# Optimization experiments

Measured on AMD Instinct MI355X. Metric: run time of the kernel, lower is better.

## Reference

```python
import jax, jax.numpy as jnp
import numpy as np

N = 100000
IN_DIM = 512
HID = (256, 256, 128)
NNZ = 3200000
SLOPE = 0.25  # leaky_relu negative slope


def _spmm(rows, cols, vals, X):
    # out[i] = sum_{e: rows[e]==i} vals[e] * X[cols[e]]  -> sparse [N,N] @ X
    return jax.ops.segment_sum(vals[:, None] * X[cols], rows, num_segments=N)


def setup_inputs() -> dict:
    key = jax.random.key(0)
    ks = jax.random.split(key, 10)
    x = jax.random.normal(ks[0], (N, IN_DIM), dtype=jnp.float32)
    adj_rows = jax.random.randint(ks[1], (NNZ,), 0, N, dtype=jnp.int32)
    adj_cols = jax.random.randint(ks[2], (NNZ,), 0, N, dtype=jnp.int32)
    adj_vals = jax.random.uniform(ks[3], (NNZ,), dtype=jnp.float32)
    # xavier_normal-ish init for weights, zeros for biases
    def xav(k, fan_in, fan_out):
        std = (2.0 / (fan_in + fan_out)) ** 0.5
        return std * jax.random.normal(k, (fan_in, fan_out), dtype=jnp.float32)
    W1 = xav(ks[4], IN_DIM, HID[0]); b1 = jnp.zeros((HID[0],), jnp.float32)
    W2 = xav(ks[5], HID[0], HID[1]); b2 = jnp.zeros((HID[1],), jnp.float32)
    W3 = xav(ks[6], HID[1], HID[2]); b3 = jnp.zeros((HID[2],), jnp.float32)
    return {"x": x, "adj_rows": adj_rows, "adj_cols": adj_cols, "adj_vals": adj_vals,
            "W1": W1, "b1": b1, "W2": W2, "b2": b2, "W3": W3, "b3": b3}


def reference(x, adj_rows, adj_cols, adj_vals, W1, b1, W2, b2, W3, b3):
    # Inference mode: F.dropout with training=False is identity.
    def layer(h, W, b):
        support = h @ W                       # dense GEMM [N, d_out]
        out = _spmm(adj_rows, adj_cols, adj_vals, support) + b
        return jax.nn.leaky_relu(out, SLOPE)
    h = layer(x, W1, b1)
    h = layer(h, W2, b2)
    h = layer(h, W3, b3)
    return h
```

## Files before the change

kernel.cpp:

```cpp
#include <hip/hip_runtime.h>

#define N_NODES 100000
#define NNZ_E   3200000
#define SLOPE   0.25f

#define NBUCK 782
#define PBLK  512
#define PCH   6250
#define CAP   6144

typedef __attribute__((ext_vector_type(8))) short bf16x8;
typedef __attribute__((ext_vector_type(4))) float f32x4;

__device__ __forceinline__ unsigned short f2b(float f) {
    union { float f; unsigned int u; } c; c.f = f;
    unsigned int u = c.u + 0x7fffu + ((c.u >> 16) & 1u);
    return (unsigned short)(u >> 16);
}
__device__ __forceinline__ float b2f_lo(unsigned int u) {
    union { unsigned int u; float f; } c; c.u = u << 16; return c.f;
}
__device__ __forceinline__ float b2f_hi(unsigned int u) {
    union { unsigned int u; float f; } c; c.u = u & 0xffff0000u; return c.f;
}

__device__ __forceinline__ void load_lds16(const unsigned short* gp, unsigned short* lp) {
    __builtin_amdgcn_global_load_lds(
        (const __attribute__((address_space(1))) void*)gp,
        (__attribute__((address_space(3))) void*)lp, 16, 0, 0);
}

__global__ __launch_bounds__(256) void partition_kernel(
    const int* __restrict__ rows, const int* __restrict__ cols,
    const float* __restrict__ vals,
    int2* __restrict__ stagedRC, float* __restrict__ stagedV,
    int* __restrict__ offs , int* __restrict__ btot)
{
    __shared__ int hist[NBUCK];
    __shared__ int ts[256];
    const int blk = blockIdx.x, t = threadIdx.x;
    const int base = blk * PCH;

    for (int i = t; i < NBUCK; i += 256) hist[i] = 0;
    __syncthreads();
    for (int e = t; e < PCH; e += 256)
        atomicAdd(&hist[rows[base + e] >> 7], 1);
    __syncthreads();

    const int i0 = t << 2;
    int c0 = (i0 + 0 < NBUCK) ? hist[i0 + 0] : 0;
    int c1 = (i0 + 1 < NBUCK) ? hist[i0 + 1] : 0;
    int c2 = (i0 + 2 < NBUCK) ? hist[i0 + 2] : 0;
    int c3 = (i0 + 3 < NBUCK) ? hist[i0 + 3] : 0;
    int s = c0 + c1 + c2 + c3;
    ts[t] = s; __syncthreads();
    for (int off = 1; off < 256; off <<= 1) {
        int u = (t >= off) ? ts[t - off] : 0;
        __syncthreads();
        ts[t] += u;
        __syncthreads();
    }
    int ex = ts[t] - s;
    int o0 = ex, o1 = ex + c0, o2 = o1 + c1, o3 = o2 + c2;
    int* gof = offs + blk * (NBUCK + 1);
    if (i0 + 0 < NBUCK) { hist[i0 + 0] = o0; gof[i0 + 0] = o0; if (c0) atomicAdd(&btot[i0 + 0], c0); }
    if (i0 + 1 < NBUCK) { hist[i0 + 1] = o1; gof[i0 + 1] = o1; if (c1) atomicAdd(&btot[i0 + 1], c1); }
    if (i0 + 2 < NBUCK) { hist[i0 + 2] = o2; gof[i0 + 2] = o2; if (c2) atomicAdd(&btot[i0 + 2], c2); }
    if (i0 + 3 < NBUCK) { hist[i0 + 3] = o3; gof[i0 + 3] = o3; if (c3) atomicAdd(&btot[i0 + 3], c3); }
    if (t == 255) gof[NBUCK] = ts[255];
    __syncthreads();

    for (int e = t; e < PCH; e += 256) {
        int r = rows[base + e];
        int p = atomicAdd(&hist[r >> 7], 1);
        stagedRC[base + p] = make_int2(r, cols[base + e]);
        stagedV[base + p] = vals[base + e];
    }
}

__global__ __launch_bounds__(1024) void bscan_kernel(const int* __restrict__ btot,
                                                     int* __restrict__ bbase,
                                                     int* __restrict__ roff) {
    __shared__ int lds[1024];
    int t = threadIdx.x;
    int v = (t < NBUCK) ? btot[t] : 0;
    lds[t] = v; __syncthreads();
    for (int off = 1; off < 1024; off <<= 1) {
        int u = (t >= off) ? lds[t - off] : 0;
        __syncthreads();
        lds[t] += u;
        __syncthreads();
    }
    if (t < NBUCK) bbase[t] = lds[t] - v;
    if (t == 0) { bbase[NBUCK] = NNZ_E; roff[N_NODES] = NNZ_E; }
}

__global__ __launch_bounds__(256) void place_kernel(
    const int* __restrict__ offs, const int* __restrict__ bbase,
    const int2* __restrict__ stagedRC, const float* __restrict__ stagedV,
    int* __restrict__ roff, int2* __restrict__ epack)
{
    __shared__ int sstart[PBLK];
    __shared__ int spos[PBLK + 1];
    __shared__ int ts[256];
    __shared__ int eCol[CAP];
    __shared__ float eVal[CAP];
    __shared__ unsigned char eRow[CAP];
    __shared__ int cnt[128];
    __shared__ int rex[128];
    const int b = blockIdx.x, t = threadIdx.x;

    for (int i = t; i < PBLK; i += 256) {
        int s = offs[i * (NBUCK + 1) + b];
        int e = offs[i * (NBUCK + 1) + b + 1];
        sstart[i] = s;
        spos[i] = e - s;
    }
    __syncthreads();
    int l0 = spos[2 * t], l1 = spos[2 * t + 1];
    int s = l0 + l1;
    ts[t] = s; __syncthreads();
    for (int off = 1; off < 256; off <<= 1) {
        int u = (t >= off) ? ts[t - off] : 0;
        __syncthreads();
        ts[t] += u;
        __syncthreads();
    }
    int ex = ts[t] - s;
    spos[2 * t] = ex; spos[2 * t + 1] = ex + l0;
    if (t == 255) spos[PBLK] = ts[255];
    __syncthreads();
    int T = spos[PBLK];
    if (T > CAP) T = CAP;

    for (int x = t; x < T; x += 256) {
        int lo = 0, hi = PBLK;
        while (hi - lo > 1) { int mid = (lo + hi) >> 1; if (spos[mid] <= x) lo = mid; else hi = mid; }
        int g = lo * PCH + sstart[lo] + (x - spos[lo]);
        int2 rc = stagedRC[g];
        eRow[x] = (unsigned char)(rc.x & 127);
        eCol[x] = rc.y;
        eVal[x] = stagedV[g];
    }
    if (t < 128) cnt[t] = 0;
    __syncthreads();
    for (int x = t; x < T; x += 256) atomicAdd(&cnt[eRow[x]], 1);
    __syncthreads();
    int cv = (t < 128) ? cnt[t] : 0;
    if (t < 128) rex[t] = cv;
    __syncthreads();
    for (int off = 1; off < 128; off <<= 1) {
        int u = (t >= off && t < 128) ? rex[t - off] : 0;
        __syncthreads();
        if (t < 128) rex[t] += u;
        __syncthreads();
    }
    const int bb = bbase[b];
    int exl = 0;
    if (t < 128) exl = rex[t] - cv;
    __syncthreads();
    if (t < 128) {
        rex[t] = exl;
        cnt[t] = 0;
        int idx = (b << 7) + t;
        if (idx < N_NODES) roff[idx] = bb + exl;
    }
    __syncthreads();
    for (int x = t; x < T; x += 256) {
        int rl = eRow[x];
        int p = bb + rex[rl] + atomicAdd(&cnt[rl], 1);
        epack[p] = make_int2(eCol[x], __float_as_int(eVal[x]));
    }
}

__global__ __launch_bounds__(256) void conv_kernel(const float* __restrict__ in,
                                                   unsigned short* __restrict__ out,
                                                   int n4) {
    int i = blockIdx.x * blockDim.x + threadIdx.x;
    if (i < n4) {
        float4 v = *(const float4*)&in[i << 2];
        ushort4 o;
        o.x = f2b(v.x); o.y = f2b(v.y); o.z = f2b(v.z); o.w = f2b(v.w);
        *(ushort4*)&out[i << 2] = o;
    }
}

__global__ __launch_bounds__(256) void wprep_kernel(const float* __restrict__ W,
                                                    unsigned short* __restrict__ Wt,
                                                    int K, int Nc) {
    int idx = blockIdx.x * blockDim.x + threadIdx.x;
    if (idx < K * Nc) {
        int n = idx / K, k = idx - n * K;
        Wt[idx] = f2b(W[(size_t)k * Nc + n]);
    }
}

__global__ __launch_bounds__(256) void gemm_bf16_128(
    const unsigned short* __restrict__ A,
    const unsigned short* __restrict__ Bt,
    unsigned short* __restrict__ C,
    int M, int K, int Nc)
{
    __shared__ __align__(16) unsigned short As[128 * 32];
    __shared__ __align__(16) unsigned short Bs[128 * 32];
    const int t = threadIdx.x;
    const int wave = t >> 6, lane = t & 63;
    const int wm = wave & 1, wn = wave >> 1;
    const int quad = lane >> 4, l16 = lane & 15;
    const int row0 = blockIdx.y * 128, col0 = blockIdx.x * 128;

    f32x4 acc[4][4];
#pragma unroll
    for (int mt = 0; mt < 4; ++mt)
#pragma unroll
        for (int nt = 0; nt < 4; ++nt) acc[mt][nt] = (f32x4){0.f, 0.f, 0.f, 0.f};

    const int sr0 = wave * 16 + (lane >> 2);
    const int sr1 = sr0 + 64;
    const int sc  = (lane & 3) << 3;

    int ra0 = row0 + sr0; if (ra0 > M - 1) ra0 = M - 1;
    int ra1 = row0 + sr1; if (ra1 > M - 1) ra1 = M - 1;
    const int rb0 = col0 + sr0;
    const int rb1 = col0 + sr1;

    for (int k0 = 0; k0 < K; k0 += 32) {
        __syncthreads();
        load_lds16(&A [(size_t)ra0 * K + k0 + sc], &As[(size_t)wave * 512]);
        load_lds16(&A [(size_t)ra1 * K + k0 + sc], &As[(size_t)(wave + 4) * 512]);
        load_lds16(&Bt[(size_t)rb0 * K + k0 + sc], &Bs[(size_t)wave * 512]);
        load_lds16(&Bt[(size_t)rb1 * K + k0 + sc], &Bs[(size_t)(wave + 4) * 512]);
        __syncthreads();

        bf16x8 af[4], bf[4];
#pragma unroll
        for (int mt = 0; mt < 4; ++mt)
            af[mt] = *(const bf16x8*)&As[(wm * 64 + mt * 16 + l16) * 32 + quad * 8];
#pragma unroll
        for (int nt = 0; nt < 4; ++nt)
            bf[nt] = *(const bf16x8*)&Bs[(wn * 64 + nt * 16 + l16) * 32 + quad * 8];
#pragma unroll
        for (int mt = 0; mt < 4; ++mt)
#pragma unroll
            for (int nt = 0; nt < 4; ++nt)
                acc[mt][nt] = __builtin_amdgcn_mfma_f32_16x16x32_bf16(
                    af[mt], bf[nt], acc[mt][nt], 0, 0, 0);
    }

#pragma unroll
    for (int mt = 0; mt < 4; ++mt)
#pragma unroll
        for (int r = 0; r < 4; ++r) {
            int row = row0 + wm * 64 + mt * 16 + quad * 4 + r;
            if (row < M) {
#pragma unroll
                for (int nt = 0; nt < 4; ++nt) {
                    int col = col0 + wn * 64 + nt * 16 + l16;
                    C[(size_t)row * Nc + col] = f2b(acc[mt][nt][r]);
                }
            }
        }
}

__global__ __launch_bounds__(256) void spmm256b_kernel(const int* __restrict__ row_off,
                                                       const int2* __restrict__ ep,
                                                       const unsigned short* __restrict__ sup,
                                                       const float* __restrict__ bias,
                                                       unsigned short* __restrict__ out) {
    int row = (blockIdx.x << 2) + (threadIdx.x >> 6);
    if (row >= N_NODES) return;
    const int lane = threadIdx.x & 63;
    const int s = row_off[row], e = row_off[row + 1];
    const int cb = lane << 2;
    float a0 = 0.f, a1 = 0.f, a2 = 0.f, a3 = 0.f;

    for (int base = s; base < e; base += 64) {
        const int idx = base + lane;
        int2 p = make_int2(0, 0);
        if (idx < e) p = ep[idx];
        const int rem = e - base;
        const int nb = (rem < 64) ? rem : 64;
        for (int jb = 0; jb < nb; jb += 8) {
#pragma unroll
            for (int j = 0; j < 8; ++j) {
                const int col = __builtin_amdgcn_readlane(p.x, jb + j);
                const float v = __int_as_float(__builtin_amdgcn_readlane(p.y, jb + j));
                const uint2 g = *(const uint2*)&sup[((size_t)col << 8) + cb];
                a0 += v * b2f_lo(g.x); a1 += v * b2f_hi(g.x);
                a2 += v * b2f_lo(g.y); a3 += v * b2f_hi(g.y);
            }
        }
    }
    float4 bv = *(const float4*)&bias[cb];
    a0 += bv.x; a1 += bv.y; a2 += bv.z; a3 += bv.w;
    a0 = (a0 >= 0.f) ? a0 : SLOPE * a0;
    a1 = (a1 >= 0.f) ? a1 : SLOPE * a1;
    a2 = (a2 >= 0.f) ? a2 : SLOPE * a2;
    a3 = (a3 >= 0.f) ? a3 : SLOPE * a3;
    ushort4 o; o.x = f2b(a0); o.y = f2b(a1); o.z = f2b(a2); o.w = f2b(a3);
    *(ushort4*)&out[((size_t)row << 8) + cb] = o;
}

__global__ __launch_bounds__(256) void spmm128f_kernel(const int* __restrict__ row_off,
                                                       const int2* __restrict__ ep,
                                                       const unsigned short* __restrict__ sup,
                                                       const float* __restrict__ bias,
                                                       float* __restrict__ out) {
    int row = (blockIdx.x << 2) + (threadIdx.x >> 6);
    if (row >= N_NODES) return;
    const int lane = threadIdx.x & 63;
    const int s = row_off[row], e = row_off[row + 1];
    const int cb = lane << 1;
    float a0 = 0.f, a1 = 0.f;

    for (int base = s; base < e; base += 64) {
        const int idx = base + lane;
        int2 p = make_int2(0, 0);
        if (idx < e) p = ep[idx];
        const int rem = e - base;
        const int nb = (rem < 64) ? rem : 64;
        for (int jb = 0; jb < nb; jb += 8) {
#pragma unroll
            for (int j = 0; j < 8; ++j) {
                const int col = __builtin_amdgcn_readlane(p.x, jb + j);
                const float v = __int_as_float(__builtin_amdgcn_readlane(p.y, jb + j));
                const unsigned int g = *(const unsigned int*)&sup[((size_t)col << 7) + cb];
                a0 += v * b2f_lo(g); a1 += v * b2f_hi(g);
            }
        }
    }
    float2 bv = *(const float2*)&bias[cb];
    a0 += bv.x; a1 += bv.y;
    a0 = (a0 >= 0.f) ? a0 : SLOPE * a0;
    a1 = (a1 >= 0.f) ? a1 : SLOPE * a1;
    *(float2*)&out[((size_t)row << 7) + cb] = make_float2(a0, a1);
}

extern "C" void kernel_launch(void* const* d_in, const int* in_sizes, int n_in,
                              void* d_out, int out_size, void* d_ws, size_t ws_size,
                              hipStream_t stream) {
    const float* x     = (const float*)d_in[0];
    const int*   arows = (const int*)d_in[1];
    const int*   acols = (const int*)d_in[2];
    const float* avals = (const float*)d_in[3];
    const float* W1 = (const float*)d_in[4];
    const float* b1 = (const float*)d_in[5];
    const float* W2 = (const float*)d_in[6];
    const float* b2 = (const float*)d_in[7];
    const float* W3 = (const float*)d_in[8];
    const float* b3 = (const float*)d_in[9];
    float* out = (float*)d_out;

    char* ws = (char*)d_ws;
    int2*  stagedRC = (int2*) (ws);
    float* stagedV  = (float*)(ws + 25600000);
    int*   offs     = (int*)  (ws + 38400000);
    int*   btot     = (int*)  (ws + 40003584);
    int*   bbase    = (int*)  (ws + 40006720);
    unsigned short* xb   = (unsigned short*)(ws);
    unsigned short* bufS = (unsigned short*)(ws + 102400000);
    unsigned short* bufH = (unsigned short*)(ws + 153600000);
    int2*  epack = (int2*)(ws + 204800000);
    int*   roff  = (int*) (ws + 230400000);
    unsigned short* Wt1 = (unsigned short*)(ws + 230800016);
    unsigned short* Wt2 = (unsigned short*)(ws + 231062160);
    unsigned short* Wt3 = (unsigned short*)(ws + 231193232);

    hipMemsetAsync(btot, 0, NBUCK * sizeof(int), stream);
    partition_kernel<<<PBLK, 256, 0, stream>>>(arows, acols, avals, stagedRC, stagedV, offs, btot);
    bscan_kernel<<<1, 1024, 0, stream>>>(btot, bbase, roff);
    place_kernel<<<NBUCK, 256, 0, stream>>>(offs, bbase, stagedRC, stagedV, roff, epack);

    wprep_kernel<<<(512 * 256 + 255) / 256, 256, 0, stream>>>(W1, Wt1, 512, 256);
    wprep_kernel<<<(256 * 256 + 255) / 256, 256, 0, stream>>>(W2, Wt2, 256, 256);
    wprep_kernel<<<(256 * 128 + 255) / 256, 256, 0, stream>>>(W3, Wt3, 256, 128);
    conv_kernel<<<(100000 * 512 / 4 + 255) / 256, 256, 0, stream>>>(x, xb, 100000 * 512 / 4);

    const int gyc = (N_NODES + 127) / 128;

    gemm_bf16_128<<<dim3(2, gyc), 256, 0, stream>>>(xb, Wt1, bufS, N_NODES, 512, 256);
    spmm256b_kernel<<<25000, 256, 0, stream>>>(roff, epack, bufS, b1, bufH);
    gemm_bf16_128<<<dim3(2, gyc), 256, 0, stream>>>(bufH, Wt2, bufS, N_NODES, 256, 256);
    spmm256b_kernel<<<25000, 256, 0, stream>>>(roff, epack, bufS, b2, bufH);
    gemm_bf16_128<<<dim3(1, gyc), 256, 0, stream>>>(bufH, Wt3, bufS, N_NODES, 256, 128);
    spmm128f_kernel<<<25000, 256, 0, stream>>>(roff, epack, bufS, b3, out);
}
```

Measured before the change: 1.191 ms.

## Fuse fp32-to-bf16 input conversion into GEMM and widen GEMM tile to 256 columns

Drops the separate conv_kernel that converted the 100000x512 fp32 input to bf16; the first GEMM now reads fp32 rows directly and packs them to bf16 into LDS. Adds a gemm256 kernel where each block covers all 256 output columns, so the A tile is loaded once rather than by two column blocks, and uses it for layers 1 and 2. The three weight-prep launches are merged into one kernel. In exchange, A for layer 1 goes through registers with fp32 global reads instead of async LDS loads, and the larger accumulator array (32 f32x4 per thread) raises register pressure and may lower occupancy.

```diff
diff --git a/kernel.cpp b/kernel.cpp
--- a/kernel.cpp
+++ b/kernel.cpp
@@ -16,6 +16,9 @@
     union { float f; unsigned int u; } c; c.f = f;
     unsigned int u = c.u + 0x7fffu + ((c.u >> 16) & 1u);
     return (unsigned short)(u >> 16);
+}
+__device__ __forceinline__ unsigned int pack2(float a, float b) {
+    return (unsigned int)f2b(a) | ((unsigned int)f2b(b) << 16);
 }
 __device__ __forceinline__ float b2f_lo(unsigned int u) {
     union { unsigned int u; float f; } c; c.u = u << 16; return c.f;
@@ -173,26 +176,111 @@
     }
 }
 
-__global__ __launch_bounds__(256) void conv_kernel(const float* __restrict__ in,
-                                                   unsigned short* __restrict__ out,
-                                                   int n4) {
-    int i = blockIdx.x * blockDim.x + threadIdx.x;
-    if (i < n4) {
-        float4 v = *(const float4*)&in[i << 2];
-        ushort4 o;
-        o.x = f2b(v.x); o.y = f2b(v.y); o.z = f2b(v.z); o.w = f2b(v.w);
-        *(ushort4*)&out[i << 2] = o;
-    }
-}
-
-__global__ __launch_bounds__(256) void wprep_kernel(const float* __restrict__ W,
-                                                    unsigned short* __restrict__ Wt,
-                                                    int K, int Nc) {
+__global__ __launch_bounds__(256) void wprep3_kernel(
+    const float* __restrict__ W1, unsigned short* __restrict__ Wt1,
+    const float* __restrict__ W2, unsigned short* __restrict__ Wt2,
+    const float* __restrict__ W3, unsigned short* __restrict__ Wt3)
+{
     int idx = blockIdx.x * blockDim.x + threadIdx.x;
-    if (idx < K * Nc) {
-        int n = idx / K, k = idx - n * K;
-        Wt[idx] = f2b(W[(size_t)k * Nc + n]);
-    }
+    if (idx < 131072) {
+        int n = idx >> 9, k = idx & 511;
+        Wt1[idx] = f2b(W1[(size_t)k * 256 + n]);
+    } else if (idx < 131072 + 65536) {
+        int i = idx - 131072;
+        int n = i >> 8, k = i & 255;
+        Wt2[i] = f2b(W2[(size_t)k * 256 + n]);
+    } else if (idx < 131072 + 65536 + 32768) {
+        int i = idx - 131072 - 65536;
+        int n = i >> 8, k = i & 255;
+        Wt3[i] = f2b(W3[(size_t)k * 128 + n]);
+    }
+}
+
+template<int AF32>
+__global__ __launch_bounds__(256) void gemm256(
+    const void* __restrict__ Av,
+    const unsigned short* __restrict__ Bt,
+    unsigned short* __restrict__ C,
+    int M, int K)
+{
+    __shared__ __align__(16) unsigned short As[128 * 32];
+    __shared__ __align__(16) unsigned short Bs[256 * 32];
+    const int t = threadIdx.x;
+    const int wave = t >> 6, lane = t & 63;
+    const int wm = wave & 1, wn = wave >> 1;
+    const int quad = lane >> 4, l16 = lane & 15;
+    const int row0 = blockIdx.x * 128;
+
+    f32x4 acc[4][8];
+#pragma unroll
+    for (int mt = 0; mt < 4; ++mt)
+#pragma unroll
+        for (int nt = 0; nt < 8; ++nt) acc[mt][nt] = (f32x4){0.f, 0.f, 0.f, 0.f};
+
+    const int sr0 = wave * 16 + (lane >> 2);
+    const int sc  = (lane & 3) << 3;
+
+    const int arow = t >> 1, ahalf = t & 1;
+    int araw = row0 + arow; if (araw > M - 1) araw = M - 1;
+    const float* Af = (const float*)Av;
+    const unsigned short* Ab = (const unsigned short*)Av;
+
+    int ra0 = row0 + sr0;      if (ra0 > M - 1) ra0 = M - 1;
+    int ra1 = row0 + sr0 + 64; if (ra1 > M - 1) ra1 = M - 1;
+
+    for (int k0 = 0; k0 < K; k0 += 32) {
+        __syncthreads();
+        if (AF32) {
+            const float* src = &Af[(size_t)araw * K + k0 + ahalf * 16];
+            float4 f0 = *(const float4*)(src + 0);
+            float4 f1 = *(const float4*)(src + 4);
+            float4 f2 = *(const float4*)(src + 8);
+            float4 f3 = *(const float4*)(src + 12);
+            uint4 lo, hi;
+            lo.x = pack2(f0.x, f0.y); lo.y = pack2(f0.z, f0.w);
+            lo.z = pack2(f1.x, f1.y); lo.w = pack2(f1.z, f1.w);
+            hi.x = pack2(f2.x, f2.y); hi.y = pack2(f2.z, f2.w);
+            hi.z = pack2(f3.x, f3.y); hi.w = pack2(f3.z, f3.w);
+            *(uint4*)&As[arow * 32 + ahalf * 16 + 0] = lo;
+            *(uint4*)&As[arow * 32 + ahalf * 16 + 8] = hi;
+        } else {
+            load_lds16(&Ab[(size_t)ra0 * K + k0 + sc], &As[(size_t)wave * 512]);
+            load_lds16(&Ab[(size_t)ra1 * K + k0 + sc], &As[(size_t)(wave + 4) * 512]);
+        }
+#pragma unroll
+        for (int g = 0; g < 4; ++g)
+            load_lds16(&Bt[(size_t)(g * 64 + sr0) * K + k0 + sc],
+                       &Bs[(size_t)(g * 4 + wave) * 512]);
+        __syncthreads();
+
+        bf16x8 af[4], bf[8];
+#pragma unroll
+        for (int mt = 0; mt < 4; ++mt)
+            af[mt] = *(const bf16x8*)&As[(wm * 64 + mt * 16 + l16) * 32 + quad * 8];
+#pragma unroll
+        for (int nt = 0; nt < 8; ++nt)
+            bf[nt] = *(const bf16x8*)&Bs[(wn * 128 + nt * 16 + l16) * 32 + quad * 8];
+#pragma unroll
+        for (int mt = 0; mt < 4; ++mt)
+#pragma unroll
+            for (int nt = 0; nt < 8; ++nt)
+                acc[mt][nt] = __builtin_amdgcn_mfma_f32_16x16x32_bf16(
+                    af[mt], bf[nt], acc[mt][nt], 0, 0, 0);
+    }
+
+#pragma unroll
+    for (int mt = 0; mt < 4; ++mt)
+#pragma unroll
+        for (int r = 0; r < 4; ++r) {
+            int row = row0 + wm * 64 + mt * 16 + quad * 4 + r;
+            if (row < M) {
+#pragma unroll
+                for (int nt = 0; nt < 8; ++nt) {
+                    int col = wn * 128 + nt * 16 + l16;
+                    C[(size_t)row * 256 + col] = f2b(acc[mt][nt][r]);
+                }
+            }
+        }
 }
 
 __global__ __launch_bounds__(256) void gemm_bf16_128(
@@ -357,7 +445,6 @@
     int*   offs     = (int*)  (ws + 38400000);
     int*   btot     = (int*)  (ws + 40003584);
     int*   bbase    = (int*)  (ws + 40006720);
-    unsigned short* xb   = (unsigned short*)(ws);
     unsigned short* bufS = (unsigned short*)(ws + 102400000);
     unsigned short* bufH = (unsigned short*)(ws + 153600000);
     int2*  epack = (int2*)(ws + 204800000);
@@ -371,16 +458,13 @@
     bscan_kernel<<<1, 1024, 0, stream>>>(btot, bbase, roff);
     place_kernel<<<NBUCK, 256, 0, stream>>>(offs, bbase, stagedRC, stagedV, roff, epack);
 
-    wprep_kernel<<<(512 * 256 + 255) / 256, 256, 0, stream>>>(W1, Wt1, 512, 256);
-    wprep_kernel<<<(256 * 256 + 255) / 256, 256, 0, stream>>>(W2, Wt2, 256, 256);
-    wprep_kernel<<<(256 * 128 + 255) / 256, 256, 0, stream>>>(W3, Wt3, 256, 128);
-    conv_kernel<<<(100000 * 512 / 4 + 255) / 256, 256, 0, stream>>>(x, xb, 100000 * 512 / 4);
+    wprep3_kernel<<<896, 256, 0, stream>>>(W1, Wt1, W2, Wt2, W3, Wt3);
 
     const int gyc = (N_NODES + 127) / 128;
 
-    gemm_bf16_128<<<dim3(2, gyc), 256, 0, stream>>>(xb, Wt1, bufS, N_NODES, 512, 256);
+    gemm256<1><<<gyc, 256, 0, stream>>>(x, Wt1, bufS, N_NODES, 512);
     spmm256b_kernel<<<25000, 256, 0, stream>>>(roff, epack, bufS, b1, bufH);
-    gemm_bf16_128<<<dim3(2, gyc), 256, 0, stream>>>(bufH, Wt2, bufS, N_NODES, 256, 256);
+    gemm256<0><<<gyc, 256, 0, stream>>>(bufH, Wt2, bufS, N_NODES, 256);
     spmm256b_kernel<<<25000, 256, 0, stream>>>(roff, epack, bufS, b2, bufH);
     gemm_bf16_128<<<dim3(1, gyc), 256, 0, stream>>>(bufH, Wt3, bufS, N_NODES, 256, 128);
     spmm128f_kernel<<<25000, 256, 0, stream>>>(roff, epack, bufS, b3, out);
```

Result: no change. 1.206 ms (+1.3%).
